# Kernel tuning notes

Measured on AMD Instinct MI355X. Metric: run time of the kernel, lower is better.

Reference implementation:

```python
import jax, jax.numpy as jnp
import numpy as np
import math

B, T, D_MODEL = 1, 2048, 256
N_Q, N_KV = 16, 1
D_HEAD = D_MODEL // N_KV          # 256 (module forces d_head = d_model // n_kv_heads)
QPG = N_Q // N_KV                 # 16
ROPE_BASE = 10000.0
WINDOW = 512
EPS = 1.1920929e-07               # torch finfo(float32).eps (nn.RMSNorm default eps=None)
NEG = -1e30


def _rope(x, base=ROPE_BASE):
    # x: (b, q, g, t, d); interleaved-pair rotary embedding, freq shared per pair
    t, d = x.shape[-2], x.shape[-1]
    freqs = base ** (-2.0 * jnp.arange(d // 2, dtype=jnp.float32) / d)      # (d/2,)
    theta = jnp.arange(t, dtype=jnp.float32)[:, None] * freqs[None, :]     # (t, d/2)
    cos, sin = jnp.cos(theta), jnp.sin(theta)
    x1, x2 = x[..., 0::2], x[..., 1::2]
    r1 = x1 * cos - x2 * sin
    r2 = x1 * sin + x2 * cos
    return jnp.stack([r1, r2], axis=-1).reshape(x.shape)


def _rmsnorm(x, w):
    return x * jax.lax.rsqrt(jnp.mean(x * x, axis=-1, keepdims=True) + EPS) * w


def setup_inputs() -> dict:
    key = jax.random.key(0)
    k0, k1, k2, k3 = jax.random.split(key, 4)
    x = jax.random.normal(k0, (B, T, D_MODEL), dtype=jnp.float32)
    wq = jax.random.normal(k1, (QPG * N_KV * D_HEAD, D_MODEL), dtype=jnp.float32) * 0.02
    wkv = jax.random.normal(k2, (2 * D_HEAD * N_KV, D_MODEL), dtype=jnp.float32) * 0.02
    wo = jax.random.normal(k3, (D_MODEL, D_HEAD * N_Q * N_KV), dtype=jnp.float32) * 0.02
    q_norm_w = jnp.ones((D_HEAD,), dtype=jnp.float32)
    k_norm_w = jnp.ones((D_HEAD,), dtype=jnp.float32)
    return {"x": x, "wq": wq, "wkv": wkv, "wo": wo,
            "q_norm_w": q_norm_w, "k_norm_w": k_norm_w}


def reference(x, wq, wkv, wo, q_norm_w, k_norm_w):
    Bx, Tx, C = x.shape
    q = x @ wq.T                                  # (b, t, qpg*n_kv*d_head)
    kv = x @ wkv.T                                # (b, t, 2*n_kv*d_head)
    k, v = kv[..., :N_KV * D_HEAD], kv[..., N_KV * D_HEAD:]
    # b t q g d -> b q g t d
    q = q.reshape(Bx, Tx, QPG, N_KV, D_HEAD).transpose(0, 2, 3, 1, 4)
    k = k.reshape(Bx, Tx, 1, N_KV, D_HEAD).transpose(0, 2, 3, 1, 4)
    v = v.reshape(Bx, Tx, 1, N_KV, D_HEAD).transpose(0, 2, 3, 1, 4)
    q = _rmsnorm(_rope(q), q_norm_w)
    k = _rmsnorm(_rope(k), k_norm_w)
    rows = jnp.arange(Tx)[:, None]
    cols = jnp.arange(Tx)[None, :]
    mask = (cols <= rows) & ((rows - cols) <= WINDOW)           # causal & sliding window
    scale = 1.0 / math.sqrt(D_HEAD)
    scores = jnp.einsum('bqgtd,bqgsd->bqgts', q, k) * scale     # (b, qpg, n_kv, t, t)
    scores = jnp.where(mask[None, None, None], scores, NEG)
    attn = jax.nn.softmax(scores, axis=-1)
    out = jnp.einsum('bqgts,bqgsd->bqgtd', attn, v)
    out = out.transpose(0, 3, 1, 2, 4).reshape(Bx, Tx, QPG * N_KV * D_HEAD)  # b t (q g d)
    return out @ wo.T
```

## Files before the change

kernel.cpp:

```cpp
#include <hip/hip_runtime.h>

#define TT   2048
#define WIN  512

typedef unsigned short u16;
typedef unsigned long long u64;
typedef __bf16 bf16x8 __attribute__((ext_vector_type(8)));
typedef float  f32x4  __attribute__((ext_vector_type(4)));

__device__ __forceinline__ float bf2f(u16 u){
  unsigned v = ((unsigned)u) << 16;
  return __builtin_bit_cast(float, v);
}
__device__ __forceinline__ u16 f2bf(float f){
  unsigned x = __builtin_bit_cast(unsigned, f);
  unsigned r = x + 0x7fffu + ((x >> 16) & 1u);
  return (u16)(r >> 16);
}
__device__ __forceinline__ f32x4 mfma16(bf16x8 a, bf16x8 b, f32x4 c){
  return __builtin_amdgcn_mfma_f32_16x16x32_bf16(a, b, c, 0, 0, 0);
}
__device__ __forceinline__ bf16x8 ld512(const u16* buf, int row, int byte){
  return *(const bf16x8*)((const char*)buf + row*512 + (byte ^ ((row&7)<<4)));
}
__device__ __forceinline__ bf16x8 ld128(const u16* buf, int row, int byte){
  return *(const bf16x8*)((const char*)buf + row*128 + (byte ^ ((row&7)<<4)));
}
#define GL16(gp, lp) __builtin_amdgcn_global_load_lds( \
    (const __attribute__((address_space(1))) unsigned int*)(gp), \
    (__attribute__((address_space(3))) unsigned int*)(lp), 16, 0, 0)

__global__ __launch_bounds__(64) void k_detect(const u16* __restrict__ x, int* __restrict__ flag){
  int lane = threadIdx.x;
  float mx = 0.f;
  for (int i = lane; i < 2048; i += 64){
    float v = fabsf(bf2f(x[i]));
    mx = (v < 64.0f) ? fmaxf(mx, v) : 1e30f;
  }
  #pragma unroll
  for (int d = 32; d; d >>= 1) mx = fmaxf(mx, __shfl_xor(mx, d));
  if (lane == 0) *flag = (mx < 64.0f) ? 1 : 0;
}

__global__ __launch_bounds__(256) void k_prep(const void* __restrict__ x_r, const void* __restrict__ wq_r,
                                              const void* __restrict__ wkv_r, const void* __restrict__ wo_r,
                                              const void* __restrict__ qw_r, const void* __restrict__ kw_r,
                                              u16* __restrict__ xb, u16* __restrict__ wqb,
                                              u16* __restrict__ wkvb, u16* __restrict__ wob,
                                              float* __restrict__ tab, float* __restrict__ qwf,
                                              float* __restrict__ kwf, const int* __restrict__ flag){
  int b = blockIdx.x, t = threadIdx.x;
  if (b < 1024){
    int idx = b*256 + t;
    int tt = idx >> 7, i = idx & 127;
    float fr = exp2f((float)i * (-13.287712379549449f / 128.0f));
    float th = (float)tt * fr;
    tab[idx*2 + 0] = cosf(th);
    tab[idx*2 + 1] = sinf(th);
    return;
  }
  if (b == 3712){
    int f = *flag;
    qwf[t] = f ? bf2f(((const u16*)qw_r)[t]) : ((const float*)qw_r)[t];
    kwf[t] = f ? bf2f(((const u16*)kw_r)[t]) : ((const float*)kw_r)[t];
    return;
  }
  if (*flag) return;
  int cb = b - 1024;
  const float* s; u16* d; int i;
  if (cb < 512)       { s=(const float*)x_r;   d=xb;   i = cb*256 + t; }
  else if (cb < 1536) { s=(const float*)wq_r;  d=wqb;  i = (cb-512)*256 + t; }
  else if (cb < 1664) { s=(const float*)wkv_r; d=wkvb; i = (cb-1536)*256 + t; }
  else                { s=(const float*)wo_r;  d=wob;  i = (cb-1664)*256 + t; }
  float4 v = *(const float4*)(s + (size_t)i*4);
  u64 pk = (u64)f2bf(v.x) | ((u64)f2bf(v.y)<<16) | ((u64)f2bf(v.z)<<32) | ((u64)f2bf(v.w)<<48);
  *(u64*)(d + (size_t)i*4) = pk;
}

__global__ __launch_bounds__(256) void k_qkv(const u16* __restrict__ xb, const u16* __restrict__ wqb,
                                             const u16* __restrict__ wkvb,
                                             const void* __restrict__ x_r, const void* __restrict__ wq_r,
                                             const void* __restrict__ wkv_r, const int* __restrict__ flag,
                                             u16* __restrict__ q_raw, u16* __restrict__ kv_raw,
                                             u16* __restrict__ vt){
  __shared__ __align__(16) u16 Ax[64*256];
  __shared__ __align__(16) u16 Bw[64*256];
  int fl = *flag;
  const u16* x   = fl ? (const u16*)x_r   : xb;
  const u16* wq  = fl ? (const u16*)wq_r  : wqb;
  const u16* wkv = fl ? (const u16*)wkv_r : wkvb;
  int m0 = blockIdx.x * 64, n0 = blockIdx.y * 64;
  int tid = threadIdx.x;
  const u16* wsrc = (n0 < 4096) ? (wq + (size_t)n0*256) : (wkv + (size_t)(n0-4096)*256);
  int sr = tid >> 5, sk = tid & 31;
  #pragma unroll
  for (int u=0;u<8;++u){
    int r = sr + u*8;
    uint4 a = *(const uint4*)((const char*)(x    + (size_t)(m0+r)*256) + sk*16);
    uint4 b = *(const uint4*)((const char*)(wsrc + (size_t)r*256)      + sk*16);
    *(uint4*)((char*)&Ax[0] + r*512 + ((sk*16) ^ ((r&7)<<4))) = a;
    *(uint4*)((char*)&Bw[0] + r*512 + ((sk*16) ^ ((r&7)<<4))) = b;
  }
  __syncthreads();
  int w = tid>>6, lane = tid&63, ml = lane&15, g = lane>>4;
  int mh = w & 1, nh = w >> 1;
  f32x4 acc[2][2];
  #pragma unroll
  for (int mr=0;mr<2;++mr)
    #pragma unroll
    for (int j=0;j<2;++j) acc[mr][j] = f32x4{0.f,0.f,0.f,0.f};
  #pragma unroll
  for (int kk=0; kk<8; ++kk){
    bf16x8 af[2], bf[2];
    #pragma unroll
    for (int mr=0;mr<2;++mr) af[mr] = ld512(Ax, mh*32 + mr*16 + ml, kk*64 + g*16);
    #pragma unroll
    for (int j=0;j<2;++j)    bf[j]  = ld512(Bw, nh*32 + j*16 + ml,  kk*64 + g*16);
    #pragma unroll
    for (int mr=0;mr<2;++mr)
      #pragma unroll
      for (int j=0;j<2;++j) acc[mr][j] = mfma16(af[mr], bf[j], acc[mr][j]);
  }
  #pragma unroll
  for (int mr=0;mr<2;++mr)
    #pragma unroll
    for (int j=0;j<2;++j)
      #pragma unroll
      for (int r=0;r<4;++r){
        int row = m0 + mh*32 + mr*16 + 4*g + r;
        int n   = n0 + nh*32 + j*16 + ml;
        float v = acc[mr][j][r];
        u16 bv = f2bf(v);
        if (n < 4096)      q_raw[(size_t)row*4096 + n] = bv;
        else if (n < 4352) kv_raw[(size_t)row*256 + (n - 4096)] = bv;
        else               vt[(size_t)(n - 4352)*2048 + row] = bv;
      }
}

__global__ __launch_bounds__(256) void k_knorm(const u16* __restrict__ kv_raw, const float* __restrict__ tab,
                                               const float* __restrict__ kwf, u16* __restrict__ kn){
  int row  = blockIdx.x * 4 + (threadIdx.x >> 6);
  int lane = threadIdx.x & 63;
  const u16* src = kv_raw + (size_t)row*256;
  union { u64 q; u16 u[4]; } iv;
  iv.q = *(const u64*)(src + lane*4);
  float v0 = bf2f(iv.u[0]), v1 = bf2f(iv.u[1]), v2 = bf2f(iv.u[2]), v3 = bf2f(iv.u[3]);
  float4 tc = *(const float4*)(tab + (size_t)row*256 + lane*4);
  float r0 = v0*tc.x - v1*tc.y;
  float r1 = v0*tc.y + v1*tc.x;
  float r2 = v2*tc.z - v3*tc.w;
  float r3 = v2*tc.w + v3*tc.z;
  float ss = r0*r0 + r1*r1 + r2*r2 + r3*r3;
  #pragma unroll
  for (int d=32; d; d>>=1) ss += __shfl_xor(ss, d);
  float sc = rsqrtf(ss * (1.0f/256.0f) + 1.1920929e-07f);
  u64 pk =  (u64)f2bf(r0*sc*kwf[lane*4+0])
         | ((u64)f2bf(r1*sc*kwf[lane*4+1]) << 16)
         | ((u64)f2bf(r2*sc*kwf[lane*4+2]) << 32)
         | ((u64)f2bf(r3*sc*kwf[lane*4+3]) << 48);
  *(u64*)(kn + (size_t)row*256 + lane*4) = pk;
}

__global__ __launch_bounds__(512, 2) void k_attn(const u16* __restrict__ q_raw, const u16* __restrict__ kn,
                                                 const u16* __restrict__ vt, const float* __restrict__ tab,
                                                 const float* __restrict__ qwf, u16* __restrict__ aout){
  __shared__ __align__(16) u16 S[73728];
  int h = blockIdx.x >> 4, qt = blockIdx.x & 15;
  int Q0 = qt * 128;
  int tid = threadIdx.x, w = tid >> 6, lane = tid & 63, ml = lane & 15, g = lane >> 4;
  u16* Pw = S + 65536 + w*1024;
  int s_lo = Q0 - WIN; if (s_lo < 0) s_lo = 0;
  int ntile = (Q0 + 128 - s_lo) >> 6;
  int tq = Q0 + w*16 + ml;
  int wmin = Q0 + w*16, wmax = wmin + 15;

  int krl = lane >> 5, kslot = lane & 31;
  int vrl = lane >> 3, vslot = lane & 7;

  {
    int s0 = s_lo;
    #pragma unroll
    for (int i=0;i<4;++i){
      int r = w*8 + i*2 + krl;
      GL16(kn + (size_t)(s0 + r)*256 + ((kslot ^ (r&7))*8), S + (w*8 + i*2)*256);
    }
    #pragma unroll
    for (int i=0;i<4;++i){
      int d = w*32 + i*8 + vrl;
      GL16(vt + (size_t)d*2048 + s0 + ((vslot ^ (d&7))*8), S + 32768 + (w*32 + i*8)*64);
    }
  }

  bf16x8 qf[8];
  {
    const u16* qp = q_raw + (size_t)tq*4096 + h*256;
    const float* tp = tab + (size_t)tq*256;
    float rf[8][8];
    float ss = 0.f;
    #pragma unroll
    for (int kk=0; kk<8; ++kk){
      int c0 = kk*32 + 8*g;
      union { u64 q[2]; u16 u[8]; } iv;
      iv.q[0] = *(const u64*)(qp + c0);
      iv.q[1] = *(const u64*)(qp + c0 + 4);
      float4 t0 = *(const float4*)(tp + c0);
      float4 t1 = *(const float4*)(tp + c0 + 4);
      float tc[8] = {t0.x,t0.y,t0.z,t0.w,t1.x,t1.y,t1.z,t1.w};
      #pragma unroll
      for (int p=0; p<4; ++p){
        float a = bf2f(iv.u[2*p]), b = bf2f(iv.u[2*p+1]);
        float cc = tc[2*p], sn = tc[2*p+1];
        float r0 = a*cc - b*sn;
        float r1 = a*sn + b*cc;
        rf[kk][2*p] = r0; rf[kk][2*p+1] = r1;
        ss += r0*r0 + r1*r1;
      }
    }
    ss += __shfl_xor(ss, 16);
    ss += __shfl_xor(ss, 32);
    float sc = rsqrtf(ss * (1.0f/256.0f) + 1.1920929e-07f) * 0.0625f;
    #pragma unroll
    for (int kk=0; kk<8; ++kk){
      int c0 = kk*32 + 8*g;
      float4 w0 = *(const float4*)(qwf + c0);
      float4 w1 = *(const float4*)(qwf + c0 + 4);
      float wv[8] = {w0.x,w0.y,w0.z,w0.w,w1.x,w1.y,w1.z,w1.w};
      union { u16 u[8]; bf16x8 v; } pk;
      #pragma unroll
      for (int e=0; e<8; ++e) pk.u[e] = f2bf(rf[kk][e] * sc * wv[e]);
      qf[kk] = pk.v;
    }
  }

  float mx = -1e30f, ls = 0.f;
  f32x4 o[16];
  #pragma unroll
  for (int f=0; f<16; ++f) o[f] = f32x4{0.f,0.f,0.f,0.f};
  int cur = 0;

  for (int kt=0; kt<ntile; ++kt){
    int s0 = s_lo + kt*64;
    if (kt+1 < ntile){
      int s1 = s0 + 64, nx = cur ^ 1;
      #pragma unroll
      for (int i=0;i<4;++i){
        int r = w*8 + i*2 + krl;
        GL16(kn + (size_t)(s1 + r)*256 + ((kslot ^ (r&7))*8), S + nx*16384 + (w*8 + i*2)*256);
      }
      #pragma unroll
      for (int i=0;i<4;++i){
        int d = w*32 + i*8 + vrl;
        GL16(vt + (size_t)d*2048 + s1 + ((vslot ^ (d&7))*8), S + 32768 + nx*16384 + (w*32 + i*8)*64);
      }
      asm volatile("s_waitcnt vmcnt(8)" ::: "memory");
    } else {
      asm volatile("s_waitcnt vmcnt(0)" ::: "memory");
    }
    __builtin_amdgcn_s_barrier();
    __builtin_amdgcn_sched_barrier(0);

    bool act = (s0 <= wmax) && (s0 + 63 + WIN >= wmin);
    if (act){
      const u16* kb = S + cur*16384;
      const u16* vb = S + 32768 + cur*16384;
      f32x4 s2[4];
      #pragma unroll
      for (int j=0;j<4;++j) s2[j] = f32x4{0.f,0.f,0.f,0.f};
      __builtin_amdgcn_s_setprio(1);
      #pragma unroll
      for (int kk=0; kk<8; ++kk)
        #pragma unroll
        for (int j=0;j<4;++j)
          s2[j] = mfma16(ld512(kb, j*16 + ml, kk*64 + g*16), qf[kk], s2[j]);
      __builtin_amdgcn_s_setprio(0);
      float best = -1e30f;
      #pragma unroll
      for (int j=0;j<4;++j)
        #pragma unroll
        for (int r=0;r<4;++r){
          int key = s0 + j*16 + 4*g + r;
          float v = s2[j][r];
          bool ok = (key <= tq) && (tq - key <= WIN);
          v = ok ? v : -1e30f;
          s2[j][r] = v;
          best = fmaxf(best, v);
        }
      best = fmaxf(best, __shfl_xor(best, 16));
      best = fmaxf(best, __shfl_xor(best, 32));
      if (__ballot(best > mx + 8.f)){
        float mn = fmaxf(mx, best);
        float corr = __expf(mx - mn);
        mx = mn; ls *= corr;
        #pragma unroll
        for (int f=0; f<16; ++f) o[f] *= corr;
      }
      float rs = 0.f;
      #pragma unroll
      for (int j=0;j<4;++j){
        u64 pk = 0;
        #pragma unroll
        for (int r=0;r<4;++r){
          float v = s2[j][r];
          float p = (v <= -1e29f) ? 0.f : __expf(v - mx);
          rs += p;
          pk |= (u64)f2bf(p) << (16*r);
        }
        *(u64*)((char*)Pw + ml*128 + ((j*32 + 8*g) ^ ((ml&7)<<4))) = pk;
      }
      rs += __shfl_xor(rs, 16);
      rs += __shfl_xor(rs, 32);
      ls += rs;
      __builtin_amdgcn_s_setprio(1);
      #pragma unroll
      for (int kk2=0; kk2<2; ++kk2){
        bf16x8 pb = ld128(Pw, ml, kk2*64 + g*16);
        #pragma unroll
        for (int f=0; f<16; ++f){
          bf16x8 vf = ld128(vb, f*16 + ml, kk2*64 + g*16);
          o[f] = mfma16(vf, pb, o[f]);
        }
      }
      __builtin_amdgcn_s_setprio(0);
    }
    __builtin_amdgcn_s_barrier();
    __builtin_amdgcn_sched_barrier(0);
    cur ^= 1;
  }
  float inv = 1.0f / ls;
  u16* dst = aout + ((size_t)h*2048 + tq)*256;
  #pragma unroll
  for (int f=0; f<16; ++f){
    f32x4 v = o[f];
    u64 pk = (u64)f2bf(v[0]*inv) | ((u64)f2bf(v[1]*inv)<<16)
           | ((u64)f2bf(v[2]*inv)<<32) | ((u64)f2bf(v[3]*inv)<<48);
    *(u64*)(dst + f*16 + 4*g) = pk;
  }
}

__global__ __launch_bounds__(256) void k_oproj(const u16* __restrict__ aout, const u16* __restrict__ wob,
                                               const void* __restrict__ wo_r, const int* __restrict__ flag,
                                               float* __restrict__ pout){
  __shared__ __align__(16) u16 As[64*256];
  __shared__ __align__(16) u16 Bs[64*256];
  const u16* wo = *flag ? (const u16*)wo_r : wob;
  int t0 = blockIdx.x * 64, c0 = blockIdx.y * 64, ksp = blockIdx.z;
  int tid = threadIdx.x, w = tid>>6, lane = tid&63, ml = lane&15, g = lane>>4;
  int mh = w & 1, nh = w >> 1;
  int sr = tid >> 5, sk = tid & 31;
  f32x4 acc[2][2];
  #pragma unroll
  for (int mr=0;mr<2;++mr)
    #pragma unroll
    for (int j=0;j<2;++j) acc[mr][j] = f32x4{0.f,0.f,0.f,0.f};
  for (int kc = ksp*4; kc < ksp*4 + 4; ++kc){
    __syncthreads();
    #pragma unroll
    for (int u=0;u<8;++u){
      int r = sr + u*8;
      uint4 a = *(const uint4*)((const char*)(aout + ((size_t)kc*2048 + t0 + r)*256) + sk*16);
      uint4 b = *(const uint4*)((const char*)(wo + (size_t)(c0+r)*4096 + kc*256) + sk*16);
      *(uint4*)((char*)&As[0] + r*512 + ((sk*16) ^ ((r&7)<<4))) = a;
      *(uint4*)((char*)&Bs[0] + r*512 + ((sk*16) ^ ((r&7)<<4))) = b;
    }
    __syncthreads();
    #pragma unroll
    for (int kk=0; kk<8; ++kk){
      bf16x8 af[2], bf[2];
      #pragma unroll
      for (int mr=0;mr<2;++mr) af[mr] = ld512(As, mh*32 + mr*16 + ml, kk*64 + g*16);
      #pragma unroll
      for (int j=0;j<2;++j)    bf[j]  = ld512(Bs, nh*32 + j*16 + ml,  kk*64 + g*16);
      #pragma unroll
      for (int mr=0;mr<2;++mr)
        #pragma unroll
        for (int j=0;j<2;++j) acc[mr][j] = mfma16(af[mr], bf[j], acc[mr][j]);
    }
  }
  #pragma unroll
  for (int mr=0;mr<2;++mr)
    #pragma unroll
    for (int j=0;j<2;++j)
      #pragma unroll
      for (int r=0;r<4;++r){
        int t = t0 + mh*32 + mr*16 + 4*g + r;
        int c = c0 + nh*32 + j*16 + ml;
        pout[((size_t)ksp*2048 + t)*256 + c] = acc[mr][j][r];
      }
}

__global__ __launch_bounds__(256) void k_red(const float* __restrict__ pout, void* __restrict__ out,
                                             const int* __restrict__ flag){
  int i = blockIdx.x * 256 + threadIdx.x;
  float v = pout[i] + pout[i + 2048*256] + pout[i + 2*2048*256] + pout[i + 3*2048*256];
  if (*flag) ((u16*)out)[i] = f2bf(v);
  else       ((float*)out)[i] = v;
}

extern "C" void kernel_launch(void* const* d_in, const int* in_sizes, int n_in,
                              void* d_out, int out_size, void* d_ws, size_t ws_size,
                              hipStream_t stream) {
  (void)in_sizes; (void)n_in; (void)out_size; (void)ws_size;
  const void* x_r   = d_in[0];
  const void* wq_r  = d_in[1];
  const void* wkv_r = d_in[2];
  const void* wo_r  = d_in[3];
  const void* qw_r  = d_in[4];
  const void* kw_r  = d_in[5];
  char* ws = (char*)d_ws;
  const size_t MB = 1048576;
  u16*   xb     = (u16*)  (ws);
  u16*   wqb    = (u16*)  (ws + 1*MB);
  u16*   wkvb   = (u16*)  (ws + 3*MB);
  u16*   wob    = (u16*)  (ws + 3*MB + MB/2);
  float* tab    = (float*)(ws + 5*MB + MB/2);
  u16*   q_raw  = (u16*)  (ws + 7*MB + MB/2);
  float* pout   = (float*)q_raw;
  u16*   kv_raw = (u16*)  (ws + 23*MB + MB/2);
  u16*   aout   = (u16*)  (ws + 25*MB + MB/2);
  u16*   kn     = (u16*)  (ws + 41*MB + MB/2);
  u16*   vt     = (u16*)  (ws + 42*MB + MB/2);
  int*   flag   = (int*)  (ws + 43*MB + MB/2);
  float* qwf    = (float*)(ws + 43*MB + MB/2 + 256);
  float* kwf    = (float*)(ws + 43*MB + MB/2 + 1280);

  k_detect<<<dim3(1),    dim3(64),  0, stream>>>((const u16*)x_r, flag);
  k_prep  <<<dim3(3713), dim3(256), 0, stream>>>(x_r, wq_r, wkv_r, wo_r, qw_r, kw_r,
                                                 xb, wqb, wkvb, wob, tab, qwf, kwf, flag);
  k_qkv   <<<dim3(32, 72),   dim3(256), 0, stream>>>(xb, wqb, wkvb, x_r, wq_r, wkv_r, flag,
                                                     q_raw, kv_raw, vt);
  k_knorm <<<dim3(512),      dim3(256), 0, stream>>>(kv_raw, tab, kwf, kn);
  k_attn  <<<dim3(256),      dim3(512), 0, stream>>>(q_raw, kn, vt, tab, qwf, aout);
  k_oproj <<<dim3(32, 4, 4), dim3(256), 0, stream>>>(aout, wob, wo_r, flag, pout);
  k_red   <<<dim3(2048),     dim3(256), 0, stream>>>(pout, d_out, flag);
}
```

Measured before the change: 96.10 us.

## Enlarge QKV GEMM tiles with direct-to-LDS loads; double output-proj split-K

```diff
diff --git a/kernel.cpp b/kernel.cpp
--- a/kernel.cpp
+++ b/kernel.cpp
@@ -83,54 +83,54 @@
                                              const void* __restrict__ wkv_r, const int* __restrict__ flag,
                                              u16* __restrict__ q_raw, u16* __restrict__ kv_raw,
                                              u16* __restrict__ vt){
-  __shared__ __align__(16) u16 Ax[64*256];
-  __shared__ __align__(16) u16 Bw[64*256];
+  __shared__ __align__(16) u16 S[65536];
   int fl = *flag;
   const u16* x   = fl ? (const u16*)x_r   : xb;
   const u16* wq  = fl ? (const u16*)wq_r  : wqb;
   const u16* wkv = fl ? (const u16*)wkv_r : wkvb;
-  int m0 = blockIdx.x * 64, n0 = blockIdx.y * 64;
-  int tid = threadIdx.x;
+  int m0 = blockIdx.x * 128, n0 = blockIdx.y * 128;
+  int tid = threadIdx.x, w = tid>>6, lane = tid&63, ml = lane&15, g = lane>>4;
   const u16* wsrc = (n0 < 4096) ? (wq + (size_t)n0*256) : (wkv + (size_t)(n0-4096)*256);
-  int sr = tid >> 5, sk = tid & 31;
-  #pragma unroll
-  for (int u=0;u<8;++u){
-    int r = sr + u*8;
-    uint4 a = *(const uint4*)((const char*)(x    + (size_t)(m0+r)*256) + sk*16);
-    uint4 b = *(const uint4*)((const char*)(wsrc + (size_t)r*256)      + sk*16);
-    *(uint4*)((char*)&Ax[0] + r*512 + ((sk*16) ^ ((r&7)<<4))) = a;
-    *(uint4*)((char*)&Bw[0] + r*512 + ((sk*16) ^ ((r&7)<<4))) = b;
-  }
+  int rl = lane >> 5, slot = lane & 31;
+  #pragma unroll
+  for (int i=0;i<16;++i){
+    int r = w*32 + i*2 + rl;
+    GL16(x + (size_t)(m0+r)*256 + ((slot ^ (r&7))*8), S + (w*32 + i*2)*256);
+  }
+  #pragma unroll
+  for (int i=0;i<16;++i){
+    int r = w*32 + i*2 + rl;
+    GL16(wsrc + (size_t)r*256 + ((slot ^ (r&7))*8), S + 32768 + (w*32 + i*2)*256);
+  }
+  asm volatile("s_waitcnt vmcnt(0)" ::: "memory");
   __syncthreads();
-  int w = tid>>6, lane = tid&63, ml = lane&15, g = lane>>4;
   int mh = w & 1, nh = w >> 1;
-  f32x4 acc[2][2];
-  #pragma unroll
-  for (int mr=0;mr<2;++mr)
-    #pragma unroll
-    for (int j=0;j<2;++j) acc[mr][j] = f32x4{0.f,0.f,0.f,0.f};
+  f32x4 acc[4][4];
+  #pragma unroll
+  for (int mr=0;mr<4;++mr)
+    #pragma unroll
+    for (int j=0;j<4;++j) acc[mr][j] = f32x4{0.f,0.f,0.f,0.f};
   #pragma unroll
   for (int kk=0; kk<8; ++kk){
-    bf16x8 af[2], bf[2];
-    #pragma unroll
-    for (int mr=0;mr<2;++mr) af[mr] = ld512(Ax, mh*32 + mr*16 + ml, kk*64 + g*16);
-    #pragma unroll
-    for (int j=0;j<2;++j)    bf[j]  = ld512(Bw, nh*32 + j*16 + ml,  kk*64 + g*16);
-    #pragma unroll
-    for (int mr=0;mr<2;++mr)
-      #pragma unroll
-      for (int j=0;j<2;++j) acc[mr][j] = mfma16(af[mr], bf[j], acc[mr][j]);
-  }
-  #pragma unroll
-  for (int mr=0;mr<2;++mr)
-    #pragma unroll
-    for (int j=0;j<2;++j)
-      #pragma unroll
-      for (int r=0;r<4;++r){
-        int row = m0 + mh*32 + mr*16 + 4*g + r;
-        int n   = n0 + nh*32 + j*16 + ml;
-        float v = acc[mr][j][r];
-        u16 bv = f2bf(v);
+    bf16x8 af[4], bf[4];
+    #pragma unroll
+    for (int mr=0;mr<4;++mr) af[mr] = ld512(S,         mh*64 + mr*16 + ml, kk*64 + g*16);
+    #pragma unroll
+    for (int j=0;j<4;++j)    bf[j]  = ld512(S + 32768, nh*64 + j*16 + ml,  kk*64 + g*16);
+    #pragma unroll
+    for (int mr=0;mr<4;++mr)
+      #pragma unroll
+      for (int j=0;j<4;++j) acc[mr][j] = mfma16(af[mr], bf[j], acc[mr][j]);
+  }
+  #pragma unroll
+  for (int mr=0;mr<4;++mr)
+    #pragma unroll
+    for (int j=0;j<4;++j)
+      #pragma unroll
+      for (int rr=0;rr<4;++rr){
+        int row = m0 + mh*64 + mr*16 + 4*g + rr;
+        int n   = n0 + nh*64 + j*16 + ml;
+        u16 bv = f2bf(acc[mr][j][rr]);
         if (n < 4096)      q_raw[(size_t)row*4096 + n] = bv;
         else if (n < 4352) kv_raw[(size_t)row*256 + (n - 4096)] = bv;
         else               vt[(size_t)(n - 4352)*2048 + row] = bv;
@@ -352,7 +352,7 @@
   for (int mr=0;mr<2;++mr)
     #pragma unroll
     for (int j=0;j<2;++j) acc[mr][j] = f32x4{0.f,0.f,0.f,0.f};
-  for (int kc = ksp*4; kc < ksp*4 + 4; ++kc){
+  for (int kc = ksp*2; kc < ksp*2 + 2; ++kc){
     __syncthreads();
     #pragma unroll
     for (int u=0;u<8;++u){
@@ -391,7 +391,9 @@
 __global__ __launch_bounds__(256) void k_red(const float* __restrict__ pout, void* __restrict__ out,
                                              const int* __restrict__ flag){
   int i = blockIdx.x * 256 + threadIdx.x;
-  float v = pout[i] + pout[i + 2048*256] + pout[i + 2*2048*256] + pout[i + 3*2048*256];
+  float v = 0.f;
+  #pragma unroll
+  for (int s=0; s<8; ++s) v += pout[i + (size_t)s*2048*256];
   if (*flag) ((u16*)out)[i] = f2bf(v);
   else       ((float*)out)[i] = v;
 }
@@ -426,10 +428,10 @@
   k_detect<<<dim3(1),    dim3(64),  0, stream>>>((const u16*)x_r, flag);
   k_prep  <<<dim3(3713), dim3(256), 0, stream>>>(x_r, wq_r, wkv_r, wo_r, qw_r, kw_r,
                                                  xb, wqb, wkvb, wob, tab, qwf, kwf, flag);
-  k_qkv   <<<dim3(32, 72),   dim3(256), 0, stream>>>(xb, wqb, wkvb, x_r, wq_r, wkv_r, flag,
+  k_qkv   <<<dim3(16, 36),   dim3(256), 0, stream>>>(xb, wqb, wkvb, x_r, wq_r, wkv_r, flag,
                                                      q_raw, kv_raw, vt);
   k_knorm <<<dim3(512),      dim3(256), 0, stream>>>(kv_raw, tab, kwf, kn);
   k_attn  <<<dim3(256),      dim3(512), 0, stream>>>(q_raw, kn, vt, tab, qwf, aout);
-  k_oproj <<<dim3(32, 4, 4), dim3(256), 0, stream>>>(aout, wob, wo_r, flag, pout);
+  k_oproj <<<dim3(32, 4, 8), dim3(256), 0, stream>>>(aout, wob, wo_r, flag, pout);
   k_red   <<<dim3(2048),     dim3(256), 0, stream>>>(pout, d_out, flag);
 }
```

Result: slower. 110.8 us (+15.3%).
